# Kernel tuning notes

Hardware: AMD Instinct MI355X
Metric: run time of the kernel (lower is better)

## Reference

```python
import jax, jax.numpy as jnp
import numpy as np


def setup_inputs() -> dict:
    key = jax.random.key(0)
    ks = jax.random.split(key, 6)
    B, T, D, E, F = 2, 2048, 1024, 8, 2048
    x = jax.random.normal(ks[0], (B, T, D), dtype=jnp.float32)
    gate_w = jax.random.normal(ks[1], (D, E), dtype=jnp.float32) * (1.0 / np.sqrt(D))
    base_w1 = jax.random.normal(ks[2], (D, F), dtype=jnp.float32) * np.sqrt(2.0 / (D + F))
    base_w2 = jax.random.normal(ks[3], (F, D), dtype=jnp.float32) * np.sqrt(2.0 / (F + D))
    expert_w1 = base_w1[None] + jax.random.normal(ks[4], (E, D, F), dtype=jnp.float32) * 0.01
    expert_w2 = base_w2[None] + jax.random.normal(ks[5], (E, F, D), dtype=jnp.float32) * 0.01
    expert_b1 = jnp.zeros((E, F), dtype=jnp.float32)
    expert_b2 = jnp.zeros((E, D), dtype=jnp.float32)
    return {"x": x, "gate_w": gate_w, "expert_w1": expert_w1, "expert_b1": expert_b1,
            "expert_w2": expert_w2, "expert_b2": expert_b2}


def reference(x, gate_w, expert_w1, expert_b1, expert_w2, expert_b2):
    # Router (TopKRouter): top-2 routing with aux load-balance loss + z-loss
    E = gate_w.shape[-1]
    TOP_K = 2
    Z_LOSS_COEF = 1e-3
    logits = jnp.einsum('btd,de->bte', x, gate_w)                       # [B,T,E]
    top_vals, top_idx = jax.lax.top_k(logits, TOP_K)                    # [B,T,K]
    router_weights = jax.nn.softmax(top_vals, axis=-1)                  # [B,T,K]
    probs = jax.nn.softmax(logits, axis=-1)
    mask = jax.nn.one_hot(top_idx[..., 0], E, dtype=x.dtype)            # top-1 expert mask
    tokens_per_expert = mask.mean(axis=(0, 1))                          # [E]
    router_prob_per_expert = probs.mean(axis=(0, 1))                    # [E]
    aux_loss = E * jnp.sum(tokens_per_expert * router_prob_per_expert) \
               + jnp.mean(logits ** 2) * Z_LOSS_COEF

    # Expert FFNs: compute all experts densely, then gather top-k outputs.
    # (Same math as per-token weight gather, without the BTDF intermediate.)
    h = jnp.einsum('btd,edf->btef', x, expert_w1) + expert_b1           # [B,T,E,F]
    h = jax.nn.gelu(h, approximate=False)                               # torch F.gelu default = erf
    out_all = jnp.einsum('btef,efd->bted', h, expert_w2) + expert_b2    # [B,T,E,D]
    gathered = jnp.take_along_axis(out_all, top_idx[..., None], axis=2) # [B,T,K,D]
    output = jnp.einsum('btk,btkd->btd', router_weights, gathered)      # [B,T,D]
    return output, aux_loss
```

## Files before the change

### kernel.cpp

```cpp
#include <hip/hip_runtime.h>
#include <hip/hip_bf16.h>

#define NTOK 4096
#define DDIM 1024
#define NEXP 8
#define FDIM 2048
#define CAP  4096
#define RTOK 16
#define MT   16

typedef float f32x4 __attribute__((ext_vector_type(4)));
typedef short s16x8 __attribute__((ext_vector_type(8)));
typedef short s16x4 __attribute__((ext_vector_type(4)));

__device__ __forceinline__ unsigned short f2bf(float f) {
  unsigned int u = __float_as_uint(f);
  unsigned int r = u + 0x7fffu + ((u >> 16) & 1u);
  return (unsigned short)(r >> 16);
}

__device__ __forceinline__ void gload16(const void* g, void* l) {
  __builtin_amdgcn_global_load_lds(
      (__attribute__((address_space(1))) unsigned int*)(g),
      (__attribute__((address_space(3))) unsigned int*)(l), 16, 0, 0);
}

__global__ __launch_bounds__(256)
void k_transpose_cast(const float* __restrict__ src, unsigned short* __restrict__ dst,
                      int R, int C) {
  __shared__ float tile[2][64][65];
  const int e = blockIdx.z;
  const int c0 = blockIdx.x * 64, r0b = blockIdx.y * 256;
  const float* s = src + (size_t)e * R * C;
  unsigned short* d = dst + (size_t)e * R * C;
  const int tid = threadIdx.x;
  const int lr = tid >> 4, lc = (tid & 15) * 4;
  const int sc = tid >> 3, sr = (tid & 7) * 8;

  float4 v[4];
  #pragma unroll
  for (int p = 0; p < 4; p++)
    v[p] = *(const float4*)(s + (size_t)(r0b + p * 16 + lr) * C + c0 + lc);

  #pragma unroll
  for (int t = 0; t < 4; t++) {
    const int cur = t & 1;
    #pragma unroll
    for (int p = 0; p < 4; p++) {
      tile[cur][p * 16 + lr][lc]     = v[p].x;
      tile[cur][p * 16 + lr][lc + 1] = v[p].y;
      tile[cur][p * 16 + lr][lc + 2] = v[p].z;
      tile[cur][p * 16 + lr][lc + 3] = v[p].w;
    }
    if (t < 3) {
      #pragma unroll
      for (int p = 0; p < 4; p++)
        v[p] = *(const float4*)(s + (size_t)(r0b + (t + 1) * 64 + p * 16 + lr) * C + c0 + lc);
    }
    __syncthreads();
    const int r0 = r0b + t * 64;
    #pragma unroll
    for (int p = 0; p < 2; p++) {
      int c = p * 32 + sc;
      s16x8 o;
      #pragma unroll
      for (int j = 0; j < 8; j++) o[j] = (short)f2bf(tile[cur][sr + j][c]);
      *(s16x8*)(d + (size_t)(c0 + c) * R + r0 + sr) = o;
    }
  }
}

__global__ __launch_bounds__(128)
void k_router(const float* __restrict__ x, const float* __restrict__ gw,
              unsigned short* __restrict__ xb,
              float* __restrict__ topw, int* __restrict__ elist,
              int* __restrict__ ecnt, int* __restrict__ cnt1,
              float* __restrict__ psum, float* __restrict__ sqsum) {
  __shared__ float gwt[NEXP][DDIM + 4];
  __shared__ float xs[RTOK][264];
  __shared__ double lgd[RTOK][NEXP];
  __shared__ float bps[NEXP];
  __shared__ int bc[NEXP];
  __shared__ float bsq;
  const int tid = threadIdx.x;
  const int tok0 = blockIdx.x * RTOK;

  for (int i = tid; i < DDIM * NEXP; i += 128) {
    int d = i >> 3, e = i & 7;
    gwt[e][d] = gw[i];
  }
  if (tid < NEXP) { bps[tid] = 0.f; bc[tid] = 0; }
  if (tid == 0) bsq = 0.f;

  const int t = tid >> 3, e = tid & 7;
  double a0 = 0.0, a1 = 0.0, a2 = 0.0, a3 = 0.0;
  for (int c = 0; c < DDIM; c += 256) {
    __syncthreads();
    for (int i = tid; i < RTOK * 64; i += 128) {
      int r = i >> 6, c4 = i & 63;
      float4 v = *(const float4*)(x + (size_t)(tok0 + r) * DDIM + c + c4 * 4);
      *(float4*)&xs[r][c4 * 4] = v;
      s16x4 o;
      o[0] = (short)f2bf(v.x); o[1] = (short)f2bf(v.y);
      o[2] = (short)f2bf(v.z); o[3] = (short)f2bf(v.w);
      *(s16x4*)(xb + (size_t)(tok0 + r) * DDIM + c + c4 * 4) = o;
    }
    __syncthreads();
    #pragma unroll 8
    for (int d4 = 0; d4 < 64; d4++) {
      float4 xv = *(const float4*)&xs[t][d4 * 4];
      float4 gv = *(const float4*)&gwt[e][c + d4 * 4];
      a0 += (double)xv.x * (double)gv.x;
      a1 += (double)xv.y * (double)gv.y;
      a2 += (double)xv.z * (double)gv.z;
      a3 += (double)xv.w * (double)gv.w;
    }
  }
  lgd[t][e] = (a0 + a1) + (a2 + a3);
  __syncthreads();

  if (tid < RTOK) {
    int tok = tok0 + tid;
    double acc[NEXP];
    #pragma unroll
    for (int k = 0; k < NEXP; k++) acc[k] = lgd[tid][k];
    int i0 = 0; double v0 = acc[0];
    #pragma unroll
    for (int k = 1; k < NEXP; k++) if (acc[k] > v0) { v0 = acc[k]; i0 = k; }
    int i1 = (i0 == 0) ? 1 : 0; double v1 = acc[i1];
    #pragma unroll
    for (int k = 0; k < NEXP; k++) if (k != i0 && acc[k] > v1) { v1 = acc[k]; i1 = k; }
    float w0 = 1.0f / (1.0f + expf((float)(v1 - v0)));
    topw[2*tok] = w0; topw[2*tok + 1] = 1.0f - w0;
    int s0 = atomicAdd(&ecnt[i0], 1); elist[i0*CAP + s0] = 2*tok;
    int s1 = atomicAdd(&ecnt[i1], 1); elist[i1*CAP + s1] = 2*tok + 1;
    atomicAdd(&bc[i0], 1);
    float lm = (float)acc[0];
    #pragma unroll
    for (int k = 1; k < NEXP; k++) lm = fmaxf(lm, (float)acc[k]);
    float pe[NEXP], ps = 0.f, sq = 0.f;
    #pragma unroll
    for (int k = 0; k < NEXP; k++) {
      float le = (float)acc[k];
      pe[k] = expf(le - lm); ps += pe[k];
      sq += le * le;
    }
    float inv = 1.0f / ps;
    #pragma unroll
    for (int k = 0; k < NEXP; k++) atomicAdd(&bps[k], pe[k] * inv);
    atomicAdd(&bsq, sq);
  }
  __syncthreads();
  if (tid < NEXP) { atomicAdd(&psum[tid], bps[tid]); atomicAdd(&cnt1[tid], bc[tid]); }
  if (tid == 0) atomicAdd(sqsum, bsq);
}

template<int K, int N, bool GELU, bool ROWSHIFT>
__global__ __launch_bounds__(512)
void k_gemm(const unsigned short* __restrict__ A, const unsigned short* __restrict__ Bt,
            const float* __restrict__ bias, void* __restrict__ Out,
            const int* __restrict__ elist, const int* __restrict__ ecnt) {
  constexpr int BM = 128, BN = 128, BK = 128, WM = 2, WN = 4;
  constexpr int GX = N / BN;
  constexpr int TOT = GX * MT * NEXP;
  constexpr int CHUNK = TOT / 8;
  constexpr int AISS = BM / 32;
  constexpr int BISS = BN / 32;
  constexpr int MF = BM / WM / 16;
  constexpr int NF = BN / WN / 16;
  __shared__ unsigned char lsA[BM * 256];
  __shared__ unsigned char lsB[BN * 256];

  const int w = blockIdx.x;
  const int swz = (w & 7) * CHUNK + (w >> 3);
  const int e = swz / (GX * MT);
  const int loc = swz % (GX * MT);
  const int mt = loc % MT, nt = loc / MT;

  const int cnt = ecnt[e];
  const int m0 = mt * BM;
  if (m0 >= cnt) return;
  const int rv = min(BM, cnt - m0);
  const int* lst = elist + e * CAP + m0;
  const int tid = threadIdx.x, wv = tid >> 6, lane = tid & 63;
  const int wm = wv / WN, wn = wv % WN;
  const unsigned short* Be = Bt + (size_t)e * N * K;

  const unsigned short* agp[AISS];
  const unsigned short* bgp[BISS];
  int adst[AISS], bdst[BISS];
  const int cu = tid & 15;
  #pragma unroll
  for (int li = 0; li < AISS; li++) {
    int r = li * 32 + (tid >> 4);
    int rr = (r < rv) ? r : 0;
    int aid = lst[rr];
    int arow = ROWSHIFT ? (aid >> 1) : aid;
    int csrc = (cu ^ (r & 15)) * 16;
    agp[li] = A + (size_t)arow * K + (csrc >> 1);
    adst[li] = r * 256 + cu * 16;
  }
  #pragma unroll
  for (int li = 0; li < BISS; li++) {
    int r = li * 32 + (tid >> 4);
    int csrc = (cu ^ (r & 15)) * 16;
    bgp[li] = Be + (size_t)(nt * BN + r) * K + (csrc >> 1);
    bdst[li] = r * 256 + cu * 16;
  }

  f32x4 acc[MF][NF];
  #pragma unroll
  for (int mi = 0; mi < MF; mi++)
    #pragma unroll
    for (int ni = 0; ni < NF; ni++)
      acc[mi][ni] = (f32x4){0.f, 0.f, 0.f, 0.f};

  constexpr int NK = K / BK;
  for (int t = 0; t < NK; ++t) {
    const int k0 = t * BK;
    #pragma unroll
    for (int li = 0; li < AISS; li++) gload16(agp[li] + k0, &lsA[adst[li]]);
    #pragma unroll
    for (int li = 0; li < BISS; li++) gload16(bgp[li] + k0, &lsB[bdst[li]]);
    __syncthreads();
    #pragma unroll
    for (int ks = 0; ks < 4; ks++) {
      s16x8 af[MF], bf[NF];
      #pragma unroll
      for (int mi = 0; mi < MF; mi++) {
        int row = wm * (BM / WM) + mi * 16 + (lane & 15);
        int c16 = (ks * 4 + (lane >> 4)) ^ (row & 15);
        af[mi] = *(const s16x8*)&lsA[row * 256 + c16 * 16];
      }
      #pragma unroll
      for (int ni = 0; ni < NF; ni++) {
        int row = wn * (BN / WN) + ni * 16 + (lane & 15);
        int c16 = (ks * 4 + (lane >> 4)) ^ (row & 15);
        bf[ni] = *(const s16x8*)&lsB[row * 256 + c16 * 16];
      }
      #pragma unroll
      for (int mi = 0; mi < MF; mi++)
        #pragma unroll
        for (int ni = 0; ni < NF; ni++)
          acc[mi][ni] = __builtin_amdgcn_mfma_f32_16x16x32_bf16(af[mi], bf[ni], acc[mi][ni], 0, 0, 0);
    }
    __syncthreads();
  }

  const int g4 = (lane >> 4) * 4, cn = lane & 15;
  #pragma unroll
  for (int mi = 0; mi < MF; mi++) {
    #pragma unroll
    for (int reg = 0; reg < 4; reg++) {
      int r = wm * (BM / WM) + mi * 16 + g4 + reg;
      if (r < rv) {
        int aid = lst[r];
        #pragma unroll
        for (int ni = 0; ni < NF; ni++) {
          int n = nt * BN + wn * (BN / WN) + ni * 16 + cn;
          float v = acc[mi][ni][reg] + bias[(size_t)e * N + n];
          if constexpr (GELU) {
            v = 0.5f * v * (1.0f + erff(v * 0.70710678118654752f));
            ((unsigned short*)Out)[(size_t)aid * N + n] = f2bf(v);
          } else {
            ((float*)Out)[(size_t)aid * N + n] = v;
          }
        }
      }
    }
  }
}

__global__ void k_combine(const float* __restrict__ buf, const float* __restrict__ topw,
                          float* __restrict__ out,
                          const int* __restrict__ cnt1, const float* __restrict__ psum,
                          const float* __restrict__ sqsum) {
  int i = blockIdx.x * 256 + threadIdx.x;
  int t = i >> 8, c = i & 255;
  float w0 = topw[2*t], w1 = topw[2*t + 1];
  float4 a = ((const float4*)(buf + (size_t)(2*t) * DDIM))[c];
  float4 b = ((const float4*)(buf + (size_t)(2*t + 1) * DDIM))[c];
  float4 o;
  o.x = w0*a.x + w1*b.x; o.y = w0*a.y + w1*b.y;
  o.z = w0*a.z + w1*b.z; o.w = w0*a.w + w1*b.w;
  ((float4*)out)[i] = o;
  if (i == 0) {
    float s = 0.f;
    for (int e = 0; e < NEXP; e++)
      s += ((float)cnt1[e] / (float)NTOK) * (psum[e] / (float)NTOK);
    out[(size_t)NTOK * DDIM] = (float)NEXP * s + (*sqsum) / (float)(NTOK * NEXP) * 1e-3f;
  }
}

extern "C" void kernel_launch(void* const* d_in, const int* in_sizes, int n_in,
                              void* d_out, int out_size, void* d_ws, size_t ws_size,
                              hipStream_t stream) {
  const float* x  = (const float*)d_in[0];
  const float* gw = (const float*)d_in[1];
  const float* w1 = (const float*)d_in[2];
  const float* b1 = (const float*)d_in[3];
  const float* w2 = (const float*)d_in[4];
  const float* b2 = (const float*)d_in[5];
  float* out = (float*)d_out;
  char* p = (char*)d_ws;

  int*   ecnt  = (int*)p;
  int*   cnt1  = (int*)(p + 32);
  float* psum  = (float*)(p + 64);
  float* sqsum = (float*)(p + 96);
  float* topw  = (float*)(p + 256);
  int*   elist = (int*)(p + 256 + 32768);
  unsigned short* xb  = (unsigned short*)(p + 256 + 32768 + 131072);
  unsigned short* w1t = xb  + (size_t)NTOK * DDIM;
  unsigned short* w2t = w1t + (size_t)NEXP * DDIM * FDIM;
  unsigned short* Hb  = w2t + (size_t)NEXP * DDIM * FDIM;
  float* obuf = (float*)(Hb + (size_t)NTOK * 2 * FDIM);

  hipMemsetAsync(p, 0, 128, stream);
  k_transpose_cast<<<dim3(FDIM/64, DDIM/256, NEXP), 256, 0, stream>>>(w1, w1t, DDIM, FDIM);
  k_transpose_cast<<<dim3(DDIM/64, FDIM/256, NEXP), 256, 0, stream>>>(w2, w2t, FDIM, DDIM);
  k_router<<<NTOK / RTOK, 128, 0, stream>>>(x, gw, xb, topw, elist, ecnt, cnt1, psum, sqsum);
  k_gemm<DDIM, FDIM, true,  true ><<<(FDIM/128)*MT*NEXP, 512, 0, stream>>>(xb, w1t, b1, Hb, elist, ecnt);
  k_gemm<FDIM, DDIM, false, false><<<(DDIM/128)*MT*NEXP, 512, 0, stream>>>(Hb, w2t, b2, obuf, elist, ecnt);
  k_combine<<<NTOK * DDIM / 4 / 256, 256, 0, stream>>>(obuf, topw, out, cnt1, psum, sqsum);
}
```

Baseline: 249.4 us.

## Double-buffer LDS in grouped expert GEMM and enlarge tiles

The grouped MoE GEMM now uses two LDS buffers with BK=64, so the next K-slice is loaded while MFMA runs on the current one. This replaces the single-buffered BK=128 loop that waited at a barrier on every load. Tile sizes become template parameters: 256x256 for the first GEMM and 128x256 for the second. The swizzle is changed to an 8-wide XOR pattern to match the new row width. Larger tiles raise register and LDS pressure, and with fewer blocks the last partially filled expert tiles can waste more work.

```diff
diff --git a/kernel.cpp b/kernel.cpp
--- a/kernel.cpp
+++ b/kernel.cpp
@@ -7,7 +7,6 @@
 #define FDIM 2048
 #define CAP  4096
 #define RTOK 16
-#define MT   16
 
 typedef float f32x4 __attribute__((ext_vector_type(4)));
 typedef short s16x8 __attribute__((ext_vector_type(8)));
@@ -155,27 +154,26 @@
   if (tid == 0) atomicAdd(sqsum, bsq);
 }
 
-template<int K, int N, bool GELU, bool ROWSHIFT>
+template<int K, int N, int BM, int BN, int MTT, bool GELU, bool ROWSHIFT>
 __global__ __launch_bounds__(512)
 void k_gemm(const unsigned short* __restrict__ A, const unsigned short* __restrict__ Bt,
             const float* __restrict__ bias, void* __restrict__ Out,
             const int* __restrict__ elist, const int* __restrict__ ecnt) {
-  constexpr int BM = 128, BN = 128, BK = 128, WM = 2, WN = 4;
+  constexpr int WM = 2, WN = 4;
   constexpr int GX = N / BN;
-  constexpr int TOT = GX * MT * NEXP;
-  constexpr int CHUNK = TOT / 8;
-  constexpr int AISS = BM / 32;
-  constexpr int BISS = BN / 32;
+  constexpr int CHUNK = GX * MTT;
+  constexpr int AISS = BM / 64;
+  constexpr int BISS = BN / 64;
   constexpr int MF = BM / WM / 16;
   constexpr int NF = BN / WN / 16;
-  __shared__ unsigned char lsA[BM * 256];
-  __shared__ unsigned char lsB[BN * 256];
+  __shared__ unsigned char lsA[2][BM * 128];
+  __shared__ unsigned char lsB[2][BN * 128];
 
   const int w = blockIdx.x;
   const int swz = (w & 7) * CHUNK + (w >> 3);
-  const int e = swz / (GX * MT);
-  const int loc = swz % (GX * MT);
-  const int mt = loc % MT, nt = loc / MT;
+  const int e = swz / CHUNK;
+  const int loc = swz % CHUNK;
+  const int mt = loc % MTT, nt = loc / MTT;
 
   const int cnt = ecnt[e];
   const int m0 = mt * BM;
@@ -189,23 +187,21 @@
   const unsigned short* agp[AISS];
   const unsigned short* bgp[BISS];
   int adst[AISS], bdst[BISS];
-  const int cu = tid & 15;
+  const int u = tid & 7;
   #pragma unroll
   for (int li = 0; li < AISS; li++) {
-    int r = li * 32 + (tid >> 4);
+    int r = li * 64 + (tid >> 3);
     int rr = (r < rv) ? r : 0;
     int aid = lst[rr];
     int arow = ROWSHIFT ? (aid >> 1) : aid;
-    int csrc = (cu ^ (r & 15)) * 16;
-    agp[li] = A + (size_t)arow * K + (csrc >> 1);
-    adst[li] = r * 256 + cu * 16;
+    agp[li] = A + (size_t)arow * K + (u ^ (r & 7)) * 8;
+    adst[li] = r * 128 + u * 16;
   }
   #pragma unroll
   for (int li = 0; li < BISS; li++) {
-    int r = li * 32 + (tid >> 4);
-    int csrc = (cu ^ (r & 15)) * 16;
-    bgp[li] = Be + (size_t)(nt * BN + r) * K + (csrc >> 1);
-    bdst[li] = r * 256 + cu * 16;
+    int r = li * 64 + (tid >> 3);
+    bgp[li] = Be + (size_t)(nt * BN + r) * K + (u ^ (r & 7)) * 8;
+    bdst[li] = r * 128 + u * 16;
   }
 
   f32x4 acc[MF][NF];
@@ -215,28 +211,35 @@
     for (int ni = 0; ni < NF; ni++)
       acc[mi][ni] = (f32x4){0.f, 0.f, 0.f, 0.f};
 
-  constexpr int NK = K / BK;
+  auto stage = [&](int kt, int b) {
+    const int k0 = kt * 64;
+    #pragma unroll
+    for (int li = 0; li < AISS; li++) gload16(agp[li] + k0, &lsA[b][adst[li]]);
+    #pragma unroll
+    for (int li = 0; li < BISS; li++) gload16(bgp[li] + k0, &lsB[b][bdst[li]]);
+  };
+
+  constexpr int NK = K / 64;
+  stage(0, 0);
+  __syncthreads();
+
+  int cur = 0;
   for (int t = 0; t < NK; ++t) {
-    const int k0 = t * BK;
-    #pragma unroll
-    for (int li = 0; li < AISS; li++) gload16(agp[li] + k0, &lsA[adst[li]]);
-    #pragma unroll
-    for (int li = 0; li < BISS; li++) gload16(bgp[li] + k0, &lsB[bdst[li]]);
-    __syncthreads();
-    #pragma unroll
-    for (int ks = 0; ks < 4; ks++) {
+    if (t + 1 < NK) stage(t + 1, cur ^ 1);
+    #pragma unroll
+    for (int ks = 0; ks < 2; ks++) {
       s16x8 af[MF], bf[NF];
       #pragma unroll
       for (int mi = 0; mi < MF; mi++) {
         int row = wm * (BM / WM) + mi * 16 + (lane & 15);
-        int c16 = (ks * 4 + (lane >> 4)) ^ (row & 15);
-        af[mi] = *(const s16x8*)&lsA[row * 256 + c16 * 16];
+        int un = (ks * 4 + (lane >> 4)) ^ (row & 7);
+        af[mi] = *(const s16x8*)&lsA[cur][row * 128 + un * 16];
       }
       #pragma unroll
       for (int ni = 0; ni < NF; ni++) {
         int row = wn * (BN / WN) + ni * 16 + (lane & 15);
-        int c16 = (ks * 4 + (lane >> 4)) ^ (row & 15);
-        bf[ni] = *(const s16x8*)&lsB[row * 256 + c16 * 16];
+        int un = (ks * 4 + (lane >> 4)) ^ (row & 7);
+        bf[ni] = *(const s16x8*)&lsB[cur][row * 128 + un * 16];
       }
       #pragma unroll
       for (int mi = 0; mi < MF; mi++)
@@ -245,6 +248,7 @@
           acc[mi][ni] = __builtin_amdgcn_mfma_f32_16x16x32_bf16(af[mi], bf[ni], acc[mi][ni], 0, 0, 0);
     }
     __syncthreads();
+    cur ^= 1;
   }
 
   const int g4 = (lane >> 4) * 4, cn = lane & 15;
@@ -320,7 +324,7 @@
   k_transpose_cast<<<dim3(FDIM/64, DDIM/256, NEXP), 256, 0, stream>>>(w1, w1t, DDIM, FDIM);
   k_transpose_cast<<<dim3(DDIM/64, FDIM/256, NEXP), 256, 0, stream>>>(w2, w2t, FDIM, DDIM);
   k_router<<<NTOK / RTOK, 128, 0, stream>>>(x, gw, xb, topw, elist, ecnt, cnt1, psum, sqsum);
-  k_gemm<DDIM, FDIM, true,  true ><<<(FDIM/128)*MT*NEXP, 512, 0, stream>>>(xb, w1t, b1, Hb, elist, ecnt);
-  k_gemm<FDIM, DDIM, false, false><<<(DDIM/128)*MT*NEXP, 512, 0, stream>>>(Hb, w2t, b2, obuf, elist, ecnt);
+  k_gemm<DDIM, FDIM, 256, 256,  8, true,  true ><<<(FDIM/256)*8*NEXP,  512, 0, stream>>>(xb, w1t, b1, Hb, elist, ecnt);
+  k_gemm<FDIM, DDIM, 128, 256, 16, false, false><<<(DDIM/256)*16*NEXP, 512, 0, stream>>>(Hb, w2t, b2, obuf, elist, ecnt);
   k_combine<<<NTOK * DDIM / 4 / 256, 256, 0, stream>>>(obuf, topw, out, cnt1, psum, sqsum);
 }
```

After: 318.6 us. +27.8%, slower.
